# Performance work log

Hardware: AMD Instinct MI355X
Metric: run time of the kernel (lower is better)

The kernel has to match this reference:

```python
import jax, jax.numpy as jnp
import numpy as np

N_REF, N_IN, D_FEAT, P, N_ELEM = 4096, 8192, 512, 256, 4


def setup_inputs() -> dict:
    key = jax.random.key(0)
    k1, k2, k3, k4, k5 = jax.random.split(key, 5)
    return {
        "Alpha": jax.random.normal(k1, (P, N_REF), dtype=jnp.float32) * 0.05,
        "X_ref": jax.random.normal(k2, (N_REF, D_FEAT), dtype=jnp.float32),
        "desc": jax.random.normal(k3, (N_IN, D_FEAT), dtype=jnp.float32),
        "Z_ref": jax.random.randint(k4, (N_REF,), 0, N_ELEM, dtype=jnp.int32),
        "Z": jax.random.randint(k5, (N_IN,), 0, N_ELEM, dtype=jnp.int32),
        "expK": 2,
    }


def reference(Alpha, X_ref, desc, Z_ref, Z, expK):
    # Per-element grouped kernel: K[i, j] = (X_ref[i] . desc[j])**expK,
    # contribution only where ref atom i and query atom j share the element.
    # This is exactly the gather -> per-element GEMM+pow -> combine -> scatter
    # of the original module, expressed as one masked dense computation.
    K = jnp.power(jnp.matmul(X_ref, desc.T), expK)          # [N_ref, N_in]
    same_elem = Z_ref[:, None] == Z[None, :]                # [N_ref, N_in]
    K_masked = jnp.where(same_elem, K, jnp.zeros((), K.dtype))
    y = jnp.matmul(Alpha, K_masked)                          # [P, N_in]
    return y
```

## Files before the change

kernel.cpp:

```cpp
#include <hip/hip_runtime.h>
#include <stdint.h>

#define P_DIM 256
#define NREF  4096
#define NIN   8192
#define DF    512
#define NE    4
#define CREF  1536
#define CIN   2560
#define AE_LD (NE * CREF)

typedef __bf16 bf16x8 __attribute__((ext_vector_type(8)));
typedef float  f32x4  __attribute__((ext_vector_type(4)));
typedef unsigned short ush8 __attribute__((ext_vector_type(8)));

static __device__ __forceinline__ unsigned short f2bf(float f) {
    uint32_t u = __builtin_bit_cast(uint32_t, f);
    u += 0x7FFFu + ((u >> 16) & 1u);
    return (unsigned short)(u >> 16);
}

__global__ __launch_bounds__(256) void plan_sort(
    const int* __restrict__ Zr, const int* __restrict__ Z,
    int* __restrict__ iperm, int* __restrict__ jperm, int* __restrict__ cnt) {
    __shared__ int histX[NE][256];
    __shared__ int histD[NE][256];
    const int t = threadIdx.x;
    constexpr int CHX = NREF / 256;
    constexpr int CHD = NIN / 256;

    int lc[NE];
#pragma unroll
    for (int e = 0; e < NE; ++e) lc[e] = 0;
    for (int k = 0; k < CHX; ++k) lc[Zr[t * CHX + k] & (NE - 1)]++;
#pragma unroll
    for (int e = 0; e < NE; ++e) histX[e][t] = lc[e];

#pragma unroll
    for (int e = 0; e < NE; ++e) lc[e] = 0;
    for (int k = 0; k < CHD; ++k) lc[Z[t * CHD + k] & (NE - 1)]++;
#pragma unroll
    for (int e = 0; e < NE; ++e) histD[e][t] = lc[e];

    __syncthreads();
    if (t < 2 * NE) {
        int b = t & (NE - 1);
        int isD = t >> 2;
        int run = 0;
        if (!isD) {
            for (int u = 0; u < 256; ++u) { int v = histX[b][u]; histX[b][u] = run; run += v; }
            cnt[b] = run;
        } else {
            for (int u = 0; u < 256; ++u) { int v = histD[b][u]; histD[b][u] = run; run += v; }
            cnt[NE + b] = run;
        }
    }
    __syncthreads();

    int off[NE];
#pragma unroll
    for (int e = 0; e < NE; ++e) off[e] = histX[e][t];
    for (int k = 0; k < CHX; ++k) {
        int i = t * CHX + k;
        int e = Zr[i] & (NE - 1);
        iperm[e * CREF + off[e]++] = i;
    }
#pragma unroll
    for (int e = 0; e < NE; ++e) off[e] = histD[e][t];
    for (int k = 0; k < CHD; ++k) {
        int j = t * CHD + k;
        int e = Z[j] & (NE - 1);
        jperm[e * CIN + off[e]++] = j;
    }
}

__global__ void gather_pad(const float* __restrict__ X_ref, const float* __restrict__ desc,
                           const int* __restrict__ iperm, const int* __restrict__ jperm,
                           const int* __restrict__ cnt,
                           unsigned short* __restrict__ Xe, unsigned short* __restrict__ De) {
    int w = (blockIdx.x * blockDim.x + threadIdx.x) >> 6;
    int lane = threadIdx.x & 63;
    const float* src = nullptr;
    unsigned short* dstp;
    if (w < NE * CREF) {
        int e = w / CREF, s = w - e * CREF;
        if (s < cnt[e]) src = X_ref + (size_t)iperm[w] * DF;
        dstp = Xe + (size_t)w * DF;
    } else {
        int w2 = w - NE * CREF;
        int e = w2 / CIN, s = w2 - e * CIN;
        if (s < cnt[NE + e]) src = desc + (size_t)jperm[w2] * DF;
        dstp = De + (size_t)w2 * DF;
    }
    ush8 o;
    if (src) {
        float4 a = *(const float4*)(src + lane * 8);
        float4 b = *(const float4*)(src + lane * 8 + 4);
        o[0] = f2bf(a.x); o[1] = f2bf(a.y); o[2] = f2bf(a.z); o[3] = f2bf(a.w);
        o[4] = f2bf(b.x); o[5] = f2bf(b.y); o[6] = f2bf(b.z); o[7] = f2bf(b.w);
    } else {
        o = (ush8){0, 0, 0, 0, 0, 0, 0, 0};
    }
    *(ush8*)(dstp + lane * 8) = o;
}

__global__ void alpha_gather(const float* __restrict__ Alpha, const int* __restrict__ iperm,
                             const int* __restrict__ cnt, unsigned short* __restrict__ Ae) {
    int idx = blockIdx.x * blockDim.x + threadIdx.x;
    int p = idx / AE_LD;
    int col = idx - p * AE_LD;
    int e = col / CREF;
    int ic = col - e * CREF;
    unsigned short v = 0;
    if (ic < cnt[e]) v = f2bf(Alpha[(size_t)p * NREF + iperm[col]]);
    Ae[idx] = v;
}

__global__ __launch_bounds__(256) void g1_grouped(
    const unsigned short* __restrict__ DeA, const unsigned short* __restrict__ XeA,
    unsigned short* __restrict__ KtA, const int* __restrict__ cnt) {
    constexpr int BK = 64;
    const int e = blockIdx.z;
    const int padR = (cnt[e] + 127) & ~127;
    const int padI = (cnt[NE + e] + 127) & ~127;
    const int m0 = blockIdx.y * 128;
    const int n0 = blockIdx.x * 128;
    if (m0 >= padI || n0 >= padR) return;

    const unsigned short* A = DeA + (size_t)e * CIN * DF;
    const unsigned short* B = XeA + (size_t)e * CREF * DF;
    unsigned short* C = KtA + (size_t)e * CIN * CREF;

    __shared__ unsigned short tA[128 * BK];
    __shared__ unsigned short tB[128 * BK];

    const int tid = threadIdx.x, wave = tid >> 6, lane = tid & 63;
    const int wr = wave >> 1, wc = wave & 1;
    const int waveM = wr * 64, waveN = wc * 64;
    const int lrow = lane >> 3, ls = lane & 7;
    const int l15 = lane & 15, lq = lane >> 4;

    f32x4 acc[4][4];
#pragma unroll
    for (int r = 0; r < 4; ++r)
#pragma unroll
        for (int c = 0; c < 4; ++c) acc[r][c] = (f32x4){0.f, 0.f, 0.f, 0.f};

#pragma unroll 1
    for (int k0 = 0; k0 < DF; k0 += BK) {
        __syncthreads();
#pragma unroll
        for (int it = 0; it < 8; ++it) {
            int cb = wave + it * 4;
            bool isB = cb >= 16;
            int cb2 = isB ? cb - 16 : cb;
            int row = cb2 * 8 + lrow;
            int g = ls ^ (row & 7);
            const unsigned short* gp = (isB ? B : A)
                + (size_t)((isB ? n0 : m0) + row) * DF + (size_t)(k0 + g * 8);
            unsigned short* lp = (isB ? tB : tA) + cb2 * (8 * BK);
            __builtin_amdgcn_global_load_lds(
                (const __attribute__((address_space(1))) void*)gp,
                (__attribute__((address_space(3))) void*)lp, 16, 0, 0);
        }
        __syncthreads();
#pragma unroll
        for (int kk = 0; kk < BK; kk += 32) {
            const int cbase = kk >> 3;
            bf16x8 af[4], bf[4];
#pragma unroll
            for (int r = 0; r < 4; ++r) {
                int m = waveM + r * 16 + l15;
                int ch = (cbase + lq) ^ (m & 7);
                af[r] = *(const bf16x8*)&tA[m * BK + ch * 8];
            }
#pragma unroll
            for (int c = 0; c < 4; ++c) {
                int n = waveN + c * 16 + l15;
                int ch = (cbase + lq) ^ (n & 7);
                bf[c] = *(const bf16x8*)&tB[n * BK + ch * 8];
            }
#pragma unroll
            for (int r = 0; r < 4; ++r)
#pragma unroll
                for (int c = 0; c < 4; ++c)
                    acc[r][c] = __builtin_amdgcn_mfma_f32_16x16x32_bf16(
                        af[r], bf[c], acc[r][c], 0, 0, 0);
        }
    }

#pragma unroll
    for (int r = 0; r < 4; ++r) {
        int mb = m0 + waveM + r * 16 + lq * 4;
#pragma unroll
        for (int reg = 0; reg < 4; ++reg) {
            size_t ro = (size_t)(mb + reg) * CREF;
#pragma unroll
            for (int c = 0; c < 4; ++c) {
                int n = n0 + waveN + c * 16 + l15;
                float v = acc[r][c][reg];
                C[ro + n] = f2bf(v * v);
            }
        }
    }
}

__global__ __launch_bounds__(256) void g2_grouped(
    const unsigned short* __restrict__ Ae, const unsigned short* __restrict__ KtA,
    const int* __restrict__ jperm, const int* __restrict__ cnt,
    float* __restrict__ out) {
    constexpr int BK = 64;
    const int e = blockIdx.z;
    const int cntI = cnt[NE + e];
    const int padR = (cnt[e] + 127) & ~127;
    const int n0 = blockIdx.x * 64;
    const int m0 = blockIdx.y * 128;
    if (n0 >= cntI) return;

    const unsigned short* B = KtA + (size_t)e * CIN * CREF;

    __shared__ unsigned short tA[128 * BK];
    __shared__ unsigned short tB[64 * BK];

    const int tid = threadIdx.x, wave = tid >> 6, lane = tid & 63;
    const int wr = wave >> 1, wc = wave & 1;
    const int waveM = wr * 64, waveN = wc * 32;
    const int lrow = lane >> 3, ls = lane & 7;
    const int l15 = lane & 15, lq = lane >> 4;

    f32x4 acc[4][2];
#pragma unroll
    for (int r = 0; r < 4; ++r)
#pragma unroll
        for (int c = 0; c < 2; ++c) acc[r][c] = (f32x4){0.f, 0.f, 0.f, 0.f};

#pragma unroll 1
    for (int k0 = 0; k0 < padR; k0 += BK) {
        __syncthreads();
#pragma unroll
        for (int it = 0; it < 6; ++it) {
            int cb = wave + it * 4;
            bool isB = cb >= 16;
            int cb2 = isB ? cb - 16 : cb;
            int row = cb2 * 8 + lrow;
            int g = ls ^ (row & 7);
            const unsigned short* gp = isB
                ? B + (size_t)(n0 + row) * CREF + (size_t)(k0 + g * 8)
                : Ae + (size_t)(m0 + row) * AE_LD + (size_t)(e * CREF + k0 + g * 8);
            unsigned short* lp = (isB ? tB : tA) + cb2 * (8 * BK);
            __builtin_amdgcn_global_load_lds(
                (const __attribute__((address_space(1))) void*)gp,
                (__attribute__((address_space(3))) void*)lp, 16, 0, 0);
        }
        __syncthreads();
#pragma unroll
        for (int kk = 0; kk < BK; kk += 32) {
            const int cbase = kk >> 3;
            bf16x8 af[4], bf[2];
#pragma unroll
            for (int r = 0; r < 4; ++r) {
                int m = waveM + r * 16 + l15;
                int ch = (cbase + lq) ^ (m & 7);
                af[r] = *(const bf16x8*)&tA[m * BK + ch * 8];
            }
#pragma unroll
            for (int c = 0; c < 2; ++c) {
                int n = waveN + c * 16 + l15;
                int ch = (cbase + lq) ^ (n & 7);
                bf[c] = *(const bf16x8*)&tB[n * BK + ch * 8];
            }
#pragma unroll
            for (int r = 0; r < 4; ++r)
#pragma unroll
                for (int c = 0; c < 2; ++c)
                    acc[r][c] = __builtin_amdgcn_mfma_f32_16x16x32_bf16(
                        af[r], bf[c], acc[r][c], 0, 0, 0);
        }
    }

    int jok[2], jdest[2];
#pragma unroll
    for (int c = 0; c < 2; ++c) {
        int jl = n0 + waveN + c * 16 + l15;
        jok[c] = jl < cntI;
        jdest[c] = jok[c] ? jperm[e * CIN + jl] : 0;
    }
#pragma unroll
    for (int r = 0; r < 4; ++r) {
        int pb = m0 + waveM + r * 16 + lq * 4;
#pragma unroll
        for (int reg = 0; reg < 4; ++reg) {
            size_t ro = (size_t)(pb + reg) * NIN;
#pragma unroll
            for (int c = 0; c < 2; ++c)
                if (jok[c]) out[ro + jdest[c]] = acc[r][c][reg];
        }
    }
}

extern "C" void kernel_launch(void* const* d_in, const int* in_sizes, int n_in,
                              void* d_out, int out_size, void* d_ws, size_t ws_size,
                              hipStream_t stream) {
    const float* Alpha = (const float*)d_in[0];
    const float* X_ref = (const float*)d_in[1];
    const float* desc  = (const float*)d_in[2];
    const int*   Z_ref = (const int*)d_in[3];
    const int*   Z     = (const int*)d_in[4];
    float* out = (float*)d_out;

    unsigned short* Xe = (unsigned short*)d_ws;
    unsigned short* De = Xe + (size_t)NE * CREF * DF;
    unsigned short* Ae = De + (size_t)NE * CIN * DF;
    unsigned short* Kt = Ae + (size_t)P_DIM * AE_LD;
    int* iperm = (int*)(Kt + (size_t)NE * CIN * CREF);
    int* jperm = iperm + NE * CREF;
    int* cnt   = jperm + NE * CIN;

    plan_sort<<<1, 256, 0, stream>>>(Z_ref, Z, iperm, jperm, cnt);

    gather_pad<<<NE * (CREF + CIN) * 64 / 256, 256, 0, stream>>>(
        X_ref, desc, iperm, jperm, cnt, Xe, De);

    alpha_gather<<<P_DIM * AE_LD / 256, 256, 0, stream>>>(Alpha, iperm, cnt, Ae);

    g1_grouped<<<dim3(CREF / 128, CIN / 128, NE), 256, 0, stream>>>(De, Xe, Kt, cnt);

    g2_grouped<<<dim3(CIN / 64, P_DIM / 128, NE), 256, 0, stream>>>(Ae, Kt, jperm, cnt, out);
}
```

Before: 150.6 us.

## Double-buffer GEMM LDS tiles, fuse gather kernels, coalesce sort reads

Both grouped GEMMs now use two LDS buffers and issue the next tile's global-to-LDS loads before computing the current one. This is meant to overlap memory latency with MFMA work, at the cost of doubled shared memory and possibly lower occupancy. The X/desc gather and the Alpha gather are merged into one launch, and the Alpha gather now writes 8 bf16 values per thread with a single vector store. The sort kernel reads Z in a strided, coalesced order, which changes the permutation order but not correctness.

```diff
diff --git a/kernel.cpp b/kernel.cpp
--- a/kernel.cpp
+++ b/kernel.cpp
@@ -32,13 +32,13 @@
     int lc[NE];
 #pragma unroll
     for (int e = 0; e < NE; ++e) lc[e] = 0;
-    for (int k = 0; k < CHX; ++k) lc[Zr[t * CHX + k] & (NE - 1)]++;
+    for (int k = 0; k < CHX; ++k) lc[Zr[t + 256 * k] & (NE - 1)]++;
 #pragma unroll
     for (int e = 0; e < NE; ++e) histX[e][t] = lc[e];
 
 #pragma unroll
     for (int e = 0; e < NE; ++e) lc[e] = 0;
-    for (int k = 0; k < CHD; ++k) lc[Z[t * CHD + k] & (NE - 1)]++;
+    for (int k = 0; k < CHD; ++k) lc[Z[t + 256 * k] & (NE - 1)]++;
 #pragma unroll
     for (int e = 0; e < NE; ++e) histD[e][t] = lc[e];
 
@@ -61,59 +61,71 @@
 #pragma unroll
     for (int e = 0; e < NE; ++e) off[e] = histX[e][t];
     for (int k = 0; k < CHX; ++k) {
-        int i = t * CHX + k;
+        int i = t + 256 * k;
         int e = Zr[i] & (NE - 1);
         iperm[e * CREF + off[e]++] = i;
     }
 #pragma unroll
     for (int e = 0; e < NE; ++e) off[e] = histD[e][t];
     for (int k = 0; k < CHD; ++k) {
-        int j = t * CHD + k;
+        int j = t + 256 * k;
         int e = Z[j] & (NE - 1);
         jperm[e * CIN + off[e]++] = j;
     }
 }
 
-__global__ void gather_pad(const float* __restrict__ X_ref, const float* __restrict__ desc,
+#define GATHER_BLOCKS (NE * (CREF + CIN) / 4)
+#define ALPHA_BLOCKS  (P_DIM * AE_LD / (256 * 8))
+
+__global__ void gather_all(const float* __restrict__ Alpha,
+                           const float* __restrict__ X_ref, const float* __restrict__ desc,
                            const int* __restrict__ iperm, const int* __restrict__ jperm,
                            const int* __restrict__ cnt,
-                           unsigned short* __restrict__ Xe, unsigned short* __restrict__ De) {
-    int w = (blockIdx.x * blockDim.x + threadIdx.x) >> 6;
-    int lane = threadIdx.x & 63;
-    const float* src = nullptr;
-    unsigned short* dstp;
-    if (w < NE * CREF) {
-        int e = w / CREF, s = w - e * CREF;
-        if (s < cnt[e]) src = X_ref + (size_t)iperm[w] * DF;
-        dstp = Xe + (size_t)w * DF;
+                           unsigned short* __restrict__ Xe, unsigned short* __restrict__ De,
+                           unsigned short* __restrict__ Ae) {
+    if (blockIdx.x < GATHER_BLOCKS) {
+        int w = (blockIdx.x * blockDim.x + threadIdx.x) >> 6;
+        int lane = threadIdx.x & 63;
+        const float* src = nullptr;
+        unsigned short* dstp;
+        if (w < NE * CREF) {
+            int e = w / CREF, s = w - e * CREF;
+            if (s < cnt[e]) src = X_ref + (size_t)iperm[w] * DF;
+            dstp = Xe + (size_t)w * DF;
+        } else {
+            int w2 = w - NE * CREF;
+            int e = w2 / CIN, s = w2 - e * CIN;
+            if (s < cnt[NE + e]) src = desc + (size_t)jperm[w2] * DF;
+            dstp = De + (size_t)w2 * DF;
+        }
+        ush8 o;
+        if (src) {
+            float4 a = *(const float4*)(src + lane * 8);
+            float4 b = *(const float4*)(src + lane * 8 + 4);
+            o[0] = f2bf(a.x); o[1] = f2bf(a.y); o[2] = f2bf(a.z); o[3] = f2bf(a.w);
+            o[4] = f2bf(b.x); o[5] = f2bf(b.y); o[6] = f2bf(b.z); o[7] = f2bf(b.w);
+        } else {
+            o = (ush8){0, 0, 0, 0, 0, 0, 0, 0};
+        }
+        *(ush8*)(dstp + lane * 8) = o;
     } else {
-        int w2 = w - NE * CREF;
-        int e = w2 / CIN, s = w2 - e * CIN;
-        if (s < cnt[NE + e]) src = desc + (size_t)jperm[w2] * DF;
-        dstp = De + (size_t)w2 * DF;
-    }
-    ush8 o;
-    if (src) {
-        float4 a = *(const float4*)(src + lane * 8);
-        float4 b = *(const float4*)(src + lane * 8 + 4);
-        o[0] = f2bf(a.x); o[1] = f2bf(a.y); o[2] = f2bf(a.z); o[3] = f2bf(a.w);
-        o[4] = f2bf(b.x); o[5] = f2bf(b.y); o[6] = f2bf(b.z); o[7] = f2bf(b.w);
-    } else {
-        o = (ush8){0, 0, 0, 0, 0, 0, 0, 0};
-    }
-    *(ush8*)(dstp + lane * 8) = o;
-}
-
-__global__ void alpha_gather(const float* __restrict__ Alpha, const int* __restrict__ iperm,
-                             const int* __restrict__ cnt, unsigned short* __restrict__ Ae) {
-    int idx = blockIdx.x * blockDim.x + threadIdx.x;
-    int p = idx / AE_LD;
-    int col = idx - p * AE_LD;
-    int e = col / CREF;
-    int ic = col - e * CREF;
-    unsigned short v = 0;
-    if (ic < cnt[e]) v = f2bf(Alpha[(size_t)p * NREF + iperm[col]]);
-    Ae[idx] = v;
+        int idx8 = (blockIdx.x - GATHER_BLOCKS) * 256 + threadIdx.x;
+        int p = idx8 / (AE_LD / 8);
+        int c8 = idx8 - p * (AE_LD / 8);
+        int col0 = c8 * 8;
+        int e = col0 / CREF;
+        int ic0 = col0 - e * CREF;
+        int cn = cnt[e];
+        const int* ip = iperm + col0;
+        ush8 v;
+#pragma unroll
+        for (int k = 0; k < 8; ++k) {
+            unsigned short r = 0;
+            if (ic0 + k < cn) r = f2bf(Alpha[(size_t)p * NREF + ip[k]]);
+            v[k] = r;
+        }
+        *(ush8*)(Ae + (size_t)idx8 * 8) = v;
+    }
 }
 
 __global__ __launch_bounds__(256) void g1_grouped(
@@ -131,8 +143,8 @@
     const unsigned short* B = XeA + (size_t)e * CREF * DF;
     unsigned short* C = KtA + (size_t)e * CIN * CREF;
 
-    __shared__ unsigned short tA[128 * BK];
-    __shared__ unsigned short tB[128 * BK];
+    __shared__ unsigned short tA[2][128 * BK];
+    __shared__ unsigned short tB[2][128 * BK];
 
     const int tid = threadIdx.x, wave = tid >> 6, lane = tid & 63;
     const int wr = wave >> 1, wc = wave & 1;
@@ -140,15 +152,7 @@
     const int lrow = lane >> 3, ls = lane & 7;
     const int l15 = lane & 15, lq = lane >> 4;
 
-    f32x4 acc[4][4];
-#pragma unroll
-    for (int r = 0; r < 4; ++r)
-#pragma unroll
-        for (int c = 0; c < 4; ++c) acc[r][c] = (f32x4){0.f, 0.f, 0.f, 0.f};
-
-#pragma unroll 1
-    for (int k0 = 0; k0 < DF; k0 += BK) {
-        __syncthreads();
+    auto stage = [&](int buf, int k0) {
 #pragma unroll
         for (int it = 0; it < 8; ++it) {
             int cb = wave + it * 4;
@@ -158,35 +162,50 @@
             int g = ls ^ (row & 7);
             const unsigned short* gp = (isB ? B : A)
                 + (size_t)((isB ? n0 : m0) + row) * DF + (size_t)(k0 + g * 8);
-            unsigned short* lp = (isB ? tB : tA) + cb2 * (8 * BK);
+            unsigned short* lp = (isB ? tB[buf] : tA[buf]) + cb2 * (8 * BK);
             __builtin_amdgcn_global_load_lds(
                 (const __attribute__((address_space(1))) void*)gp,
                 (__attribute__((address_space(3))) void*)lp, 16, 0, 0);
         }
-        __syncthreads();
+    };
+
+    f32x4 acc[4][4];
+#pragma unroll
+    for (int r = 0; r < 4; ++r)
+#pragma unroll
+        for (int c = 0; c < 4; ++c) acc[r][c] = (f32x4){0.f, 0.f, 0.f, 0.f};
+
+    stage(0, 0);
+    __syncthreads();
+    int buf = 0;
+#pragma unroll 1
+    for (int k0 = 0; k0 < DF; k0 += BK) {
+        if (k0 + BK < DF) stage(buf ^ 1, k0 + BK);
 #pragma unroll
         for (int kk = 0; kk < BK; kk += 32) {
             const int cbase = kk >> 3;
-            bf16x8 af[4], bf[4];
+            bf16x8 af[4], bfr[4];
 #pragma unroll
             for (int r = 0; r < 4; ++r) {
                 int m = waveM + r * 16 + l15;
                 int ch = (cbase + lq) ^ (m & 7);
-                af[r] = *(const bf16x8*)&tA[m * BK + ch * 8];
+                af[r] = *(const bf16x8*)&tA[buf][m * BK + ch * 8];
             }
 #pragma unroll
             for (int c = 0; c < 4; ++c) {
                 int n = waveN + c * 16 + l15;
                 int ch = (cbase + lq) ^ (n & 7);
-                bf[c] = *(const bf16x8*)&tB[n * BK + ch * 8];
+                bfr[c] = *(const bf16x8*)&tB[buf][n * BK + ch * 8];
             }
 #pragma unroll
             for (int r = 0; r < 4; ++r)
 #pragma unroll
                 for (int c = 0; c < 4; ++c)
                     acc[r][c] = __builtin_amdgcn_mfma_f32_16x16x32_bf16(
-                        af[r], bf[c], acc[r][c], 0, 0, 0);
-        }
+                        af[r], bfr[c], acc[r][c], 0, 0, 0);
+        }
+        __syncthreads();
+        buf ^= 1;
     }
 
 #pragma unroll
@@ -219,8 +238,8 @@
 
     const unsigned short* B = KtA + (size_t)e * CIN * CREF;
 
-    __shared__ unsigned short tA[128 * BK];
-    __shared__ unsigned short tB[64 * BK];
+    __shared__ unsigned short tA[2][128 * BK];
+    __shared__ unsigned short tB[2][64 * BK];
 
     const int tid = threadIdx.x, wave = tid >> 6, lane = tid & 63;
     const int wr = wave >> 1, wc = wave & 1;
@@ -228,15 +247,7 @@
     const int lrow = lane >> 3, ls = lane & 7;
     const int l15 = lane & 15, lq = lane >> 4;
 
-    f32x4 acc[4][2];
-#pragma unroll
-    for (int r = 0; r < 4; ++r)
-#pragma unroll
-        for (int c = 0; c < 2; ++c) acc[r][c] = (f32x4){0.f, 0.f, 0.f, 0.f};
-
-#pragma unroll 1
-    for (int k0 = 0; k0 < padR; k0 += BK) {
-        __syncthreads();
+    auto stage = [&](int buf, int k0) {
 #pragma unroll
         for (int it = 0; it < 6; ++it) {
             int cb = wave + it * 4;
@@ -247,34 +258,51 @@
             const unsigned short* gp = isB
                 ? B + (size_t)(n0 + row) * CREF + (size_t)(k0 + g * 8)
                 : Ae + (size_t)(m0 + row) * AE_LD + (size_t)(e * CREF + k0 + g * 8);
-            unsigned short* lp = (isB ? tB : tA) + cb2 * (8 * BK);
+            unsigned short* lp = (isB ? tB[buf] : tA[buf]) + cb2 * (8 * BK);
             __builtin_amdgcn_global_load_lds(
                 (const __attribute__((address_space(1))) void*)gp,
                 (__attribute__((address_space(3))) void*)lp, 16, 0, 0);
         }
+    };
+
+    f32x4 acc[4][2];
+#pragma unroll
+    for (int r = 0; r < 4; ++r)
+#pragma unroll
+        for (int c = 0; c < 2; ++c) acc[r][c] = (f32x4){0.f, 0.f, 0.f, 0.f};
+
+    if (padR > 0) {
+        stage(0, 0);
         __syncthreads();
-#pragma unroll
-        for (int kk = 0; kk < BK; kk += 32) {
-            const int cbase = kk >> 3;
-            bf16x8 af[4], bf[2];
-#pragma unroll
-            for (int r = 0; r < 4; ++r) {
-                int m = waveM + r * 16 + l15;
-                int ch = (cbase + lq) ^ (m & 7);
-                af[r] = *(const bf16x8*)&tA[m * BK + ch * 8];
+        int buf = 0;
+#pragma unroll 1
+        for (int k0 = 0; k0 < padR; k0 += BK) {
+            if (k0 + BK < padR) stage(buf ^ 1, k0 + BK);
+#pragma unroll
+            for (int kk = 0; kk < BK; kk += 32) {
+                const int cbase = kk >> 3;
+                bf16x8 af[4], bfr[2];
+#pragma unroll
+                for (int r = 0; r < 4; ++r) {
+                    int m = waveM + r * 16 + l15;
+                    int ch = (cbase + lq) ^ (m & 7);
+                    af[r] = *(const bf16x8*)&tA[buf][m * BK + ch * 8];
+                }
+#pragma unroll
+                for (int c = 0; c < 2; ++c) {
+                    int n = waveN + c * 16 + l15;
+                    int ch = (cbase + lq) ^ (n & 7);
+                    bfr[c] = *(const bf16x8*)&tB[buf][n * BK + ch * 8];
+                }
+#pragma unroll
+                for (int r = 0; r < 4; ++r)
+#pragma unroll
+                    for (int c = 0; c < 2; ++c)
+                        acc[r][c] = __builtin_amdgcn_mfma_f32_16x16x32_bf16(
+                            af[r], bfr[c], acc[r][c], 0, 0, 0);
             }
-#pragma unroll
-            for (int c = 0; c < 2; ++c) {
-                int n = waveN + c * 16 + l15;
-                int ch = (cbase + lq) ^ (n & 7);
-                bf[c] = *(const bf16x8*)&tB[n * BK + ch * 8];
-            }
-#pragma unroll
-            for (int r = 0; r < 4; ++r)
-#pragma unroll
-                for (int c = 0; c < 2; ++c)
-                    acc[r][c] = __builtin_amdgcn_mfma_f32_16x16x32_bf16(
-                        af[r], bf[c], acc[r][c], 0, 0, 0);
+            __syncthreads();
+            buf ^= 1;
         }
     }
 
@@ -318,10 +346,8 @@
 
     plan_sort<<<1, 256, 0, stream>>>(Z_ref, Z, iperm, jperm, cnt);
 
-    gather_pad<<<NE * (CREF + CIN) * 64 / 256, 256, 0, stream>>>(
-        X_ref, desc, iperm, jperm, cnt, Xe, De);
-
-    alpha_gather<<<P_DIM * AE_LD / 256, 256, 0, stream>>>(Alpha, iperm, cnt, Ae);
+    gather_all<<<GATHER_BLOCKS + ALPHA_BLOCKS, 256, 0, stream>>>(
+        Alpha, X_ref, desc, iperm, jperm, cnt, Xe, De, Ae);
 
     g1_grouped<<<dim3(CREF / 128, CIN / 128, NE), 256, 0, stream>>>(De, Xe, Kt, cnt);
 
```

Measured after the change: 157.9 us. +4.9%, slower.
